# Kernel optimization log

Measured on AMD Instinct MI355X. Metric: run time of the kernel, lower is better.

## Reference

```python
import jax, jax.numpy as jnp
import numpy as np

B, S, H, I, E, K = 1, 2048, 1024, 2048, 8, 2


def setup_inputs() -> dict:
    key = jax.random.key(0)
    k0, k1, k2, k3, k4 = jax.random.split(key, 5)
    x = jax.random.normal(k0, (B, S, H), dtype=jnp.float32)
    Wg = jax.random.normal(k1, (H, E), dtype=jnp.float32) * 0.02   # gate (no bias)
    W1 = jax.random.normal(k2, (E, H, I), dtype=jnp.float32) * 0.02  # expert up
    W3 = jax.random.normal(k3, (E, H, I), dtype=jnp.float32) * 0.02  # expert gate
    W2 = jax.random.normal(k4, (E, I, H), dtype=jnp.float32) * 0.02  # expert down
    return {"x": x, "Wg": Wg, "W1": W1, "W2": W2, "W3": W3}


def reference(x, Wg, W1, W2, W3):
    b, s, h = x.shape
    e = Wg.shape[1]
    xf = x.reshape(-1, h)                      # (T, H)
    T = xf.shape[0]

    # Router: top-2 logits, softmax over the 2 selected logits (fp32), cast back.
    logits = xf @ Wg                           # (T, E)
    top_vals, top_idx = jax.lax.top_k(logits, K)
    rw = jax.nn.softmax(top_vals.astype(jnp.float32), axis=-1).astype(x.dtype)  # (T, K)

    # Dense per-expert combine weight: w[t, e] = routing weight if expert e selected, else 0.
    w = jnp.zeros((T, e), dtype=x.dtype).at[jnp.arange(T)[:, None], top_idx].add(rw)

    # Expert MLPs computed for all experts, zero-weighted tokens contribute nothing
    # (mathematically identical to the gather/MLP/scatter-add in the torch loop).
    up = jnp.einsum('th,ehi->tei', xf, W1)     # (T, E, I)
    gate = jnp.einsum('th,ehi->tei', xf, W3)   # (T, E, I)
    act = jax.nn.silu(up) * gate               # (T, E, I)
    out = jnp.einsum('tei,eih,te->th', act, W2, w)  # (T, H)
    return out.reshape(b, s, h)
```

## Files before the change

kernel.cpp:

```cpp
#include <hip/hip_runtime.h>
#include <math.h>

#define NUM_TOK 2048
#define HDIM 1024
#define IDIM 2048
#define NEXP 8
#define MAX_ROWS 5120
#define NTM 40

typedef __attribute__((ext_vector_type(8))) short bf16x8;
typedef __attribute__((ext_vector_type(4))) float f32x4;

#define OFF_IDX   0u
#define OFF_RW    16384u
#define OFF_CNT   32768u
#define OFF_SEG   32832u
#define OFF_ROWS  33024u
#define OFF_POS   53504u
#define OFF_XB    131072u
#define OFF_W1T   8388608u
#define OFF_W3T   41943040u
#define OFF_W2T   75497472u
#define OFF_ACT   109051904u
#define OFF_SO    8388608u

__device__ __forceinline__ unsigned short f2bf(float f) {
  union { float f; unsigned u; } v; v.f = f;
  unsigned r = v.u + 0x7FFF + ((v.u >> 16) & 1);
  return (unsigned short)(r >> 16);
}

__device__ __forceinline__ void gld16(const void* g, void* l) {
  __builtin_amdgcn_global_load_lds(
      (const __attribute__((address_space(1))) void*)g,
      (__attribute__((address_space(3))) void*)l, 16, 0, 0);
}

__global__ void __launch_bounds__(256, 4)
k_prep(const float* __restrict__ W1, const float* __restrict__ W3,
       const float* __restrict__ W2,
       unsigned short* __restrict__ W1T,
       unsigned short* __restrict__ W3T,
       unsigned short* __restrict__ W2T,
       const float* __restrict__ x, const float* __restrict__ wg,
       unsigned short* __restrict__ xb,
       int* __restrict__ idx, float* __restrict__ rw) {
  __shared__ unsigned D[64 * 129];
  const int z = blockIdx.z;
  const int t = threadIdx.x;
  if (z >= 24) {
    const int wave = t >> 6, lane = t & 63;
    const int id = blockIdx.x + 32 * blockIdx.y + 256 * (z - 24);
    const int tok = id * 4 + wave;
    if (tok >= NUM_TOK) return;
    const float2* __restrict__ xr = (const float2*)(x + (size_t)tok * HDIM);
    unsigned* __restrict__ xbr = (unsigned*)(xb + (size_t)tok * HDIM);
    float acc[8];
#pragma unroll
    for (int q = 0; q < 8; ++q) acc[q] = 0.f;
#pragma unroll
    for (int j = 0; j < 8; ++j) {
      const int h2 = lane + (j << 6);
      const float2 v = xr[h2];
      const float* wrow = wg + (size_t)h2 * 16;
      const float4 a0 = *(const float4*)(wrow);
      const float4 a1 = *(const float4*)(wrow + 4);
      const float4 b0 = *(const float4*)(wrow + 8);
      const float4 b1 = *(const float4*)(wrow + 12);
      acc[0] = fmaf(v.x, a0.x, fmaf(v.y, b0.x, acc[0]));
      acc[1] = fmaf(v.x, a0.y, fmaf(v.y, b0.y, acc[1]));
      acc[2] = fmaf(v.x, a0.z, fmaf(v.y, b0.z, acc[2]));
      acc[3] = fmaf(v.x, a0.w, fmaf(v.y, b0.w, acc[3]));
      acc[4] = fmaf(v.x, a1.x, fmaf(v.y, b1.x, acc[4]));
      acc[5] = fmaf(v.x, a1.y, fmaf(v.y, b1.y, acc[5]));
      acc[6] = fmaf(v.x, a1.z, fmaf(v.y, b1.z, acc[6]));
      acc[7] = fmaf(v.x, a1.w, fmaf(v.y, b1.w, acc[7]));
      xbr[h2] = (unsigned)f2bf(v.x) | ((unsigned)f2bf(v.y) << 16);
    }
#pragma unroll
    for (int q = 0; q < 8; ++q) {
#pragma unroll
      for (int off = 32; off >= 1; off >>= 1)
        acc[q] += __shfl_xor(acc[q], off, 64);
    }
    if (lane == 0) {
      int i0 = 0; float v0 = acc[0];
#pragma unroll
      for (int q = 1; q < 8; ++q)
        if (acc[q] > v0) { v0 = acc[q]; i0 = q; }
      int i1 = -1; float v1 = -3.4e38f;
#pragma unroll
      for (int q = 0; q < 8; ++q)
        if (q != i0 && acc[q] > v1) { v1 = acc[q]; i1 = q; }
      const float e1 = expf(v1 - v0);
      const float inv = 1.f / (1.f + e1);
      idx[2 * tok] = i0; idx[2 * tok + 1] = i1;
      rw[2 * tok] = inv; rw[2 * tok + 1] = e1 * inv;
    }
    return;
  }
  const float* src; unsigned short* dst; int R, C, eidx;
  if (z < 8)       { src = W1; dst = W1T; R = HDIM; C = IDIM; eidx = z; }
  else if (z < 16) { src = W3; dst = W3T; R = HDIM; C = IDIM; eidx = z - 8; }
  else             { src = W2; dst = W2T; R = IDIM; C = HDIM; eidx = z - 16; }
  const int r0 = blockIdx.y * 256;
  const int c0 = blockIdx.x * 64;
  if (r0 >= R || c0 >= C) return;
  const size_t base = (size_t)eidx * R * C;
  const int c4 = (t & 15) * 4;
  const int r2a = t >> 4;
  float4 va[4][2][2];
#pragma unroll
  for (int p = 0; p < 4; ++p)
#pragma unroll
    for (int h = 0; h < 2; ++h) {
      const int r = r0 + p * 64 + 2 * (r2a + 16 * h);
      va[p][h][0] = *(const float4*)(src + base + (size_t)r * C + c0 + c4);
      va[p][h][1] = *(const float4*)(src + base + (size_t)(r + 1) * C + c0 + c4);
    }
  __builtin_amdgcn_sched_barrier(0);
#pragma unroll
  for (int p = 0; p < 4; ++p)
#pragma unroll
    for (int h = 0; h < 2; ++h) {
      const int r2 = p * 32 + r2a + 16 * h;
      const float4 v0 = va[p][h][0], v1 = va[p][h][1];
      const float a0[4] = {v0.x, v0.y, v0.z, v0.w};
      const float a1[4] = {v1.x, v1.y, v1.z, v1.w};
#pragma unroll
      for (int q = 0; q < 4; ++q)
        D[(c4 + q) * 129 + r2] = (unsigned)f2bf(a0[q]) | ((unsigned)f2bf(a1[q]) << 16);
    }
  __syncthreads();
  const int rq = (t & 31) * 4;
#pragma unroll
  for (int g = 0; g < 8; ++g) {
    const int c = (t >> 5) + g * 8;
    uint4 u;
    u.x = D[c * 129 + rq];
    u.y = D[c * 129 + rq + 1];
    u.z = D[c * 129 + rq + 2];
    u.w = D[c * 129 + rq + 3];
    *(uint4*)(dst + base + (size_t)(c0 + c) * R + r0 + rq * 2) = u;
  }
}

__global__ void k_segscatter(const int* __restrict__ idx, int* __restrict__ seg,
                             int* __restrict__ rowsv, int* __restrict__ pos) {
  __shared__ int hist[NEXP], cur[NEXP], sseg[NEXP];
  const int tid = threadIdx.x;
  if (tid < NEXP) { hist[tid] = 0; cur[tid] = 0; }
  __syncthreads();
  for (int s = tid; s < 2 * NUM_TOK; s += 256) atomicAdd(&hist[idx[s]], 1);
  for (int r = tid; r < MAX_ROWS; r += 256) rowsv[r] = -1;
  __syncthreads();
  if (tid == 0) {
    int s = 0;
    for (int q = 0; q < NEXP; ++q) {
      seg[q] = s; sseg[q] = s;
      s += ((hist[q] + 127) / 128) * 128;
    }
    seg[NEXP] = s;
  }
  __syncthreads();
  for (int s = tid; s < 2 * NUM_TOK; s += 256) {
    const int e = idx[s];
    const int p = atomicAdd(&cur[e], 1);
    const int rr = sseg[e] + p;
    rowsv[rr] = s;
    pos[s] = rr;
  }
}

__launch_bounds__(256, 2)
__global__ void k_gemm1(const unsigned short* __restrict__ xb,
                        const unsigned short* __restrict__ W1T,
                        const unsigned short* __restrict__ W3T,
                        const int* __restrict__ seg, const int* __restrict__ rowsv,
                        unsigned short* __restrict__ act) {
  __shared__ __align__(16) unsigned short As[2][128 * 32];
  __shared__ __align__(16) unsigned short Bs[2][128 * 32];
  const int tid = threadIdx.x;
  const int w = tid >> 6, l = tid & 63;
  const int m0 = blockIdx.y * 128;
  const int total = seg[NEXP];
  if (m0 >= total) return;
  int e = 0;
#pragma unroll
  for (int q = 1; q < NEXP; ++q) if (m0 >= seg[q]) e = q;
  const int n0 = blockIdx.x * 64;

  const int swzst = ((l & 3) ^ ((l >> 3) & 3)) * 8;
  size_t aOff[2], bOff[2];
#pragma unroll
  for (int q = 0; q < 2; ++q) {
    const int r = rowsv[m0 + w * 32 + q * 16 + (l >> 2)];
    const int tk = (r < 0) ? 0 : (r >> 1);
    aOff[q] = (size_t)tk * HDIM + swzst;
    bOff[q] = ((size_t)e * IDIM + n0 + (w & 1) * 32 + q * 16 + (l >> 2)) * HDIM + swzst;
  }
  const unsigned short* __restrict__ WT = (w < 2) ? W1T : W3T;

  f32x4 acc[2][8];
#pragma unroll
  for (int m = 0; m < 2; ++m)
#pragma unroll
    for (int nf = 0; nf < 8; ++nf) acc[m][nf] = (f32x4)0.f;

  auto stage = [&](int buf, int k0) {
#pragma unroll
    for (int q = 0; q < 2; ++q) {
      gld16(xb + aOff[q] + k0, &As[buf][(w * 32 + q * 16) * 32]);
      gld16(WT + bOff[q] + k0, &Bs[buf][(w * 32 + q * 16) * 32]);
    }
  };

  stage(0, 0);
  __syncthreads();
  const int rslot = ((l >> 4) ^ ((l >> 1) & 3)) * 8;
  const int arow = (w * 32 + (l & 15)) * 32 + rslot;
  for (int t = 0; t < HDIM / 32; ++t) {
    const int cur = t & 1;
    if (t + 1 < HDIM / 32) stage(cur ^ 1, (t + 1) * 32);
    const bf16x8 a0 = *(const bf16x8*)&As[cur][arow];
    const bf16x8 a1 = *(const bf16x8*)&As[cur][arow + 16 * 32];
#pragma unroll
    for (int nf = 0; nf < 8; ++nf) {
      const bf16x8 b = *(const bf16x8*)&Bs[cur][(nf * 16 + (l & 15)) * 32 + rslot];
      acc[0][nf] = __builtin_amdgcn_mfma_f32_16x16x32_bf16(a0, b, acc[0][nf], 0, 0, 0);
      acc[1][nf] = __builtin_amdgcn_mfma_f32_16x16x32_bf16(a1, b, acc[1][nf], 0, 0, 0);
    }
    __syncthreads();
  }
  const int rbase = m0 + w * 32 + (l >> 4) * 4;
  const int cbase = n0 + (l & 15);
#pragma unroll
  for (int m = 0; m < 2; ++m)
#pragma unroll
    for (int p = 0; p < 4; ++p) {
      const f32x4 up = acc[m][p];
      const f32x4 gt = acc[m][p + 4];
#pragma unroll
      for (int r = 0; r < 4; ++r) {
        const float u = up[r];
        const float s = (u / (1.f + expf(-u))) * gt[r];
        act[(size_t)(rbase + m * 16 + r) * IDIM + cbase + p * 16] = f2bf(s);
      }
    }
}

__launch_bounds__(256, 2)
__global__ void k_gemm2(const unsigned short* __restrict__ act,
                        const unsigned short* __restrict__ W2T,
                        const int* __restrict__ seg,
                        float* __restrict__ so) {
  __shared__ __align__(16) unsigned short As[2][128 * 32];
  __shared__ __align__(16) unsigned short Bs[2][128 * 32];
  const int tid = threadIdx.x;
  const int w = tid >> 6, l = tid & 63;
  const int m0 = blockIdx.y * 128;
  const int total = seg[NEXP];
  if (m0 >= total) return;
  int e = 0;
#pragma unroll
  for (int q = 1; q < NEXP; ++q) if (m0 >= seg[q]) e = q;
  const int n0 = blockIdx.x * 128;
  const int swz = ((tid & 3) ^ ((tid >> 3) & 3)) * 8;
  size_t aOff[2], bOff[2];
#pragma unroll
  for (int q = 0; q < 2; ++q) {
    aOff[q] = (size_t)(m0 + q * 64 + (tid >> 2)) * IDIM + swz;
    bOff[q] = ((size_t)e * HDIM + n0 + q * 64 + (tid >> 2)) * IDIM + swz;
  }

  f32x4 acc[2][8];
#pragma unroll
  for (int mf = 0; mf < 2; ++mf)
#pragma unroll
    for (int nf = 0; nf < 8; ++nf) acc[mf][nf] = (f32x4)0.f;

  auto stage = [&](int buf, int k0) {
#pragma unroll
    for (int q = 0; q < 2; ++q) {
      gld16(act + aOff[q] + k0, &As[buf][(q * 64 + (tid >> 2)) * 32 + (tid & 3) * 8]);
      gld16(W2T + bOff[q] + k0, &Bs[buf][(q * 64 + (tid >> 2)) * 32 + (tid & 3) * 8]);
    }
  };

  stage(0, 0);
  __syncthreads();
  const int rslot = ((l >> 4) ^ ((l >> 1) & 3)) * 8;
  const int arow = (w * 32 + (l & 15)) * 32 + rslot;
  for (int t = 0; t < IDIM / 32; ++t) {
    const int cur = t & 1;
    if (t + 1 < IDIM / 32) stage(cur ^ 1, (t + 1) * 32);
    const bf16x8 a0 = *(const bf16x8*)&As[cur][arow];
    const bf16x8 a1 = *(const bf16x8*)&As[cur][arow + 16 * 32];
#pragma unroll
    for (int nf = 0; nf < 8; ++nf) {
      const bf16x8 b = *(const bf16x8*)&Bs[cur][(nf * 16 + (l & 15)) * 32 + rslot];
      acc[0][nf] = __builtin_amdgcn_mfma_f32_16x16x32_bf16(a0, b, acc[0][nf], 0, 0, 0);
      acc[1][nf] = __builtin_amdgcn_mfma_f32_16x16x32_bf16(a1, b, acc[1][nf], 0, 0, 0);
    }
    __syncthreads();
  }
  const int rbase = m0 + w * 32 + (l >> 4) * 4;
  const int cbase = n0 + (l & 15);
#pragma unroll
  for (int mf = 0; mf < 2; ++mf)
#pragma unroll
    for (int nf = 0; nf < 8; ++nf)
#pragma unroll
      for (int r = 0; r < 4; ++r)
        so[(size_t)(rbase + mf * 16 + r) * HDIM + cbase + nf * 16] = acc[mf][nf][r];
}

__global__ void k_combine(const float* __restrict__ so, const int* __restrict__ pos,
                          const float* __restrict__ rw, float* __restrict__ out) {
  const int t = blockIdx.x, i = threadIdx.x;
  const int p0 = pos[2 * t], p1 = pos[2 * t + 1];
  const float w0 = rw[2 * t], w1 = rw[2 * t + 1];
  const float4 a = ((const float4*)(so + (size_t)p0 * HDIM))[i];
  const float4 b = ((const float4*)(so + (size_t)p1 * HDIM))[i];
  float4 o;
  o.x = w0 * a.x + w1 * b.x;
  o.y = w0 * a.y + w1 * b.y;
  o.z = w0 * a.z + w1 * b.z;
  o.w = w0 * a.w + w1 * b.w;
  ((float4*)(out + (size_t)t * HDIM))[i] = o;
}

extern "C" void kernel_launch(void* const* d_in, const int* in_sizes, int n_in,
                              void* d_out, int out_size, void* d_ws, size_t ws_size,
                              hipStream_t stream) {
  const float* x  = (const float*)d_in[0];
  const float* Wg = (const float*)d_in[1];
  const float* W1 = (const float*)d_in[2];
  const float* W2 = (const float*)d_in[3];
  const float* W3 = (const float*)d_in[4];
  float* out = (float*)d_out;
  char* ws = (char*)d_ws;
  int*   idx  = (int*)(ws + OFF_IDX);
  float* rw   = (float*)(ws + OFF_RW);
  int*   seg  = (int*)(ws + OFF_SEG);
  int*   rowsv= (int*)(ws + OFF_ROWS);
  int*   pos  = (int*)(ws + OFF_POS);
  unsigned short* xb  = (unsigned short*)(ws + OFF_XB);
  unsigned short* W1T = (unsigned short*)(ws + OFF_W1T);
  unsigned short* W3T = (unsigned short*)(ws + OFF_W3T);
  unsigned short* W2T = (unsigned short*)(ws + OFF_W2T);
  unsigned short* act = (unsigned short*)(ws + OFF_ACT);
  float* so = (float*)(ws + OFF_SO);

  k_prep<<<dim3(32, 8, 26), 256, 0, stream>>>(W1, W3, W2, W1T, W3T, W2T,
                                              x, Wg, xb, idx, rw);
  k_segscatter<<<1, 256, 0, stream>>>(idx, seg, rowsv, pos);
  k_gemm1<<<dim3(IDIM / 64, NTM), 256, 0, stream>>>(xb, W1T, W3T, seg, rowsv, act);
  k_gemm2<<<dim3(HDIM / 128, NTM), 256, 0, stream>>>(act, W2T, seg, so);
  k_combine<<<NUM_TOK, 256, 0, stream>>>(so, pos, rw, out);
}
```

Baseline: 186.8 us.

## Fuse fp32-to-bf16 weight conversion into GEMM B-tile staging, drop prep transpose

Removes the separate prep pass that converted and transposed all expert weights to bf16 in workspace. Both GEMMs now read fp32 weights directly into registers, pack them to bf16 and write them into a swizzled, transposed LDS layout while the MFMAs on the current buffer run. The router becomes its own small kernel. This avoids writing and re-reading about 100 MB of bf16 weights, at the cost of each GEMM block reading fp32 weights redundantly across M-tiles, more VALU and LDS-store work in the inner loop, and more register pressure.

```diff
diff --git a/kernel.cpp b/kernel.cpp
--- a/kernel.cpp
+++ b/kernel.cpp
@@ -13,14 +13,10 @@
 
 #define OFF_IDX   0u
 #define OFF_RW    16384u
-#define OFF_CNT   32768u
 #define OFF_SEG   32832u
 #define OFF_ROWS  33024u
 #define OFF_POS   53504u
 #define OFF_XB    131072u
-#define OFF_W1T   8388608u
-#define OFF_W3T   41943040u
-#define OFF_W2T   75497472u
 #define OFF_ACT   109051904u
 #define OFF_SO    8388608u
 
@@ -30,118 +26,65 @@
   return (unsigned short)(r >> 16);
 }
 
+__device__ __forceinline__ unsigned pk2(float lo, float hi) {
+  return (unsigned)f2bf(lo) | ((unsigned)f2bf(hi) << 16);
+}
+
 __device__ __forceinline__ void gld16(const void* g, void* l) {
   __builtin_amdgcn_global_load_lds(
       (const __attribute__((address_space(1))) void*)g,
       (__attribute__((address_space(3))) void*)l, 16, 0, 0);
 }
 
-__global__ void __launch_bounds__(256, 4)
-k_prep(const float* __restrict__ W1, const float* __restrict__ W3,
-       const float* __restrict__ W2,
-       unsigned short* __restrict__ W1T,
-       unsigned short* __restrict__ W3T,
-       unsigned short* __restrict__ W2T,
-       const float* __restrict__ x, const float* __restrict__ wg,
-       unsigned short* __restrict__ xb,
-       int* __restrict__ idx, float* __restrict__ rw) {
-  __shared__ unsigned D[64 * 129];
-  const int z = blockIdx.z;
-  const int t = threadIdx.x;
-  if (z >= 24) {
-    const int wave = t >> 6, lane = t & 63;
-    const int id = blockIdx.x + 32 * blockIdx.y + 256 * (z - 24);
-    const int tok = id * 4 + wave;
-    if (tok >= NUM_TOK) return;
-    const float2* __restrict__ xr = (const float2*)(x + (size_t)tok * HDIM);
-    unsigned* __restrict__ xbr = (unsigned*)(xb + (size_t)tok * HDIM);
-    float acc[8];
-#pragma unroll
-    for (int q = 0; q < 8; ++q) acc[q] = 0.f;
-#pragma unroll
-    for (int j = 0; j < 8; ++j) {
-      const int h2 = lane + (j << 6);
-      const float2 v = xr[h2];
-      const float* wrow = wg + (size_t)h2 * 16;
-      const float4 a0 = *(const float4*)(wrow);
-      const float4 a1 = *(const float4*)(wrow + 4);
-      const float4 b0 = *(const float4*)(wrow + 8);
-      const float4 b1 = *(const float4*)(wrow + 12);
-      acc[0] = fmaf(v.x, a0.x, fmaf(v.y, b0.x, acc[0]));
-      acc[1] = fmaf(v.x, a0.y, fmaf(v.y, b0.y, acc[1]));
-      acc[2] = fmaf(v.x, a0.z, fmaf(v.y, b0.z, acc[2]));
-      acc[3] = fmaf(v.x, a0.w, fmaf(v.y, b0.w, acc[3]));
-      acc[4] = fmaf(v.x, a1.x, fmaf(v.y, b1.x, acc[4]));
-      acc[5] = fmaf(v.x, a1.y, fmaf(v.y, b1.y, acc[5]));
-      acc[6] = fmaf(v.x, a1.z, fmaf(v.y, b1.z, acc[6]));
-      acc[7] = fmaf(v.x, a1.w, fmaf(v.y, b1.w, acc[7]));
-      xbr[h2] = (unsigned)f2bf(v.x) | ((unsigned)f2bf(v.y) << 16);
-    }
-#pragma unroll
-    for (int q = 0; q < 8; ++q) {
-#pragma unroll
-      for (int off = 32; off >= 1; off >>= 1)
-        acc[q] += __shfl_xor(acc[q], off, 64);
-    }
-    if (lane == 0) {
-      int i0 = 0; float v0 = acc[0];
-#pragma unroll
-      for (int q = 1; q < 8; ++q)
-        if (acc[q] > v0) { v0 = acc[q]; i0 = q; }
-      int i1 = -1; float v1 = -3.4e38f;
-#pragma unroll
-      for (int q = 0; q < 8; ++q)
-        if (q != i0 && acc[q] > v1) { v1 = acc[q]; i1 = q; }
-      const float e1 = expf(v1 - v0);
-      const float inv = 1.f / (1.f + e1);
-      idx[2 * tok] = i0; idx[2 * tok + 1] = i1;
-      rw[2 * tok] = inv; rw[2 * tok + 1] = e1 * inv;
-    }
-    return;
-  }
-  const float* src; unsigned short* dst; int R, C, eidx;
-  if (z < 8)       { src = W1; dst = W1T; R = HDIM; C = IDIM; eidx = z; }
-  else if (z < 16) { src = W3; dst = W3T; R = HDIM; C = IDIM; eidx = z - 8; }
-  else             { src = W2; dst = W2T; R = IDIM; C = HDIM; eidx = z - 16; }
-  const int r0 = blockIdx.y * 256;
-  const int c0 = blockIdx.x * 64;
-  if (r0 >= R || c0 >= C) return;
-  const size_t base = (size_t)eidx * R * C;
-  const int c4 = (t & 15) * 4;
-  const int r2a = t >> 4;
-  float4 va[4][2][2];
-#pragma unroll
-  for (int p = 0; p < 4; ++p)
-#pragma unroll
-    for (int h = 0; h < 2; ++h) {
-      const int r = r0 + p * 64 + 2 * (r2a + 16 * h);
-      va[p][h][0] = *(const float4*)(src + base + (size_t)r * C + c0 + c4);
-      va[p][h][1] = *(const float4*)(src + base + (size_t)(r + 1) * C + c0 + c4);
-    }
-  __builtin_amdgcn_sched_barrier(0);
-#pragma unroll
-  for (int p = 0; p < 4; ++p)
-#pragma unroll
-    for (int h = 0; h < 2; ++h) {
-      const int r2 = p * 32 + r2a + 16 * h;
-      const float4 v0 = va[p][h][0], v1 = va[p][h][1];
-      const float a0[4] = {v0.x, v0.y, v0.z, v0.w};
-      const float a1[4] = {v1.x, v1.y, v1.z, v1.w};
-#pragma unroll
-      for (int q = 0; q < 4; ++q)
-        D[(c4 + q) * 129 + r2] = (unsigned)f2bf(a0[q]) | ((unsigned)f2bf(a1[q]) << 16);
-    }
-  __syncthreads();
-  const int rq = (t & 31) * 4;
-#pragma unroll
-  for (int g = 0; g < 8; ++g) {
-    const int c = (t >> 5) + g * 8;
-    uint4 u;
-    u.x = D[c * 129 + rq];
-    u.y = D[c * 129 + rq + 1];
-    u.z = D[c * 129 + rq + 2];
-    u.w = D[c * 129 + rq + 3];
-    *(uint4*)(dst + base + (size_t)(c0 + c) * R + r0 + rq * 2) = u;
+
+__global__ void k_router(const float* __restrict__ x, const float* __restrict__ wg,
+                         unsigned short* __restrict__ xb,
+                         int* __restrict__ idx, float* __restrict__ rw) {
+  const int wave = threadIdx.x >> 6, lane = threadIdx.x & 63;
+  const int t = blockIdx.x * 4 + wave;
+  const float2* __restrict__ xr = (const float2*)(x + (size_t)t * HDIM);
+  unsigned* __restrict__ xbr = (unsigned*)(xb + (size_t)t * HDIM);
+  float acc[8];
+#pragma unroll
+  for (int q = 0; q < 8; ++q) acc[q] = 0.f;
+#pragma unroll
+  for (int j = 0; j < 8; ++j) {
+    const int h2 = lane + (j << 6);
+    const float2 v = xr[h2];
+    const float* wrow = wg + (size_t)h2 * 16;
+    const float4 a0 = *(const float4*)(wrow);
+    const float4 a1 = *(const float4*)(wrow + 4);
+    const float4 b0 = *(const float4*)(wrow + 8);
+    const float4 b1 = *(const float4*)(wrow + 12);
+    acc[0] = fmaf(v.x, a0.x, fmaf(v.y, b0.x, acc[0]));
+    acc[1] = fmaf(v.x, a0.y, fmaf(v.y, b0.y, acc[1]));
+    acc[2] = fmaf(v.x, a0.z, fmaf(v.y, b0.z, acc[2]));
+    acc[3] = fmaf(v.x, a0.w, fmaf(v.y, b0.w, acc[3]));
+    acc[4] = fmaf(v.x, a1.x, fmaf(v.y, b1.x, acc[4]));
+    acc[5] = fmaf(v.x, a1.y, fmaf(v.y, b1.y, acc[5]));
+    acc[6] = fmaf(v.x, a1.z, fmaf(v.y, b1.z, acc[6]));
+    acc[7] = fmaf(v.x, a1.w, fmaf(v.y, b1.w, acc[7]));
+    xbr[h2] = pk2(v.x, v.y);
+  }
+#pragma unroll
+  for (int q = 0; q < 8; ++q) {
+#pragma unroll
+    for (int off = 32; off >= 1; off >>= 1)
+      acc[q] += __shfl_xor(acc[q], off, 64);
+  }
+  if (lane == 0) {
+    int i0 = 0; float v0 = acc[0];
+#pragma unroll
+    for (int q = 1; q < 8; ++q)
+      if (acc[q] > v0) { v0 = acc[q]; i0 = q; }
+    int i1 = -1; float v1 = -3.4e38f;
+#pragma unroll
+    for (int q = 0; q < 8; ++q)
+      if (q != i0 && acc[q] > v1) { v1 = acc[q]; i1 = q; }
+    const float e1 = expf(v1 - v0);
+    const float inv = 1.f / (1.f + e1);
+    idx[2 * t] = i0; idx[2 * t + 1] = i1;
+    rw[2 * t] = inv; rw[2 * t + 1] = e1 * inv;
   }
 }
 
@@ -174,8 +117,8 @@
 
 __launch_bounds__(256, 2)
 __global__ void k_gemm1(const unsigned short* __restrict__ xb,
-                        const unsigned short* __restrict__ W1T,
-                        const unsigned short* __restrict__ W3T,
+                        const float* __restrict__ W1f,
+                        const float* __restrict__ W3f,
                         const int* __restrict__ seg, const int* __restrict__ rowsv,
                         unsigned short* __restrict__ act) {
   __shared__ __align__(16) unsigned short As[2][128 * 32];
@@ -190,16 +133,45 @@
   for (int q = 1; q < NEXP; ++q) if (m0 >= seg[q]) e = q;
   const int n0 = blockIdx.x * 64;
 
-  const int swzst = ((l & 3) ^ ((l >> 3) & 3)) * 8;
-  size_t aOff[2], bOff[2];
+  const int swzA = ((l & 3) ^ ((l >> 4) & 3) ^ ((l >> 3) & 3)) * 8;
+  size_t aOff[2];
 #pragma unroll
   for (int q = 0; q < 2; ++q) {
     const int r = rowsv[m0 + w * 32 + q * 16 + (l >> 2)];
     const int tk = (r < 0) ? 0 : (r >> 1);
-    aOff[q] = (size_t)tk * HDIM + swzst;
-    bOff[q] = ((size_t)e * IDIM + n0 + (w & 1) * 32 + q * 16 + (l >> 2)) * HDIM + swzst;
-  }
-  const unsigned short* __restrict__ WT = (w < 2) ? W1T : W3T;
+    aOff[q] = (size_t)tk * HDIM + swzA;
+  }
+  const int kk = tid >> 4;
+  const int ng = tid & 15;
+  const size_t bBase = (size_t)e * HDIM * IDIM + (size_t)(2 * kk) * IDIM + n0 + ng * 4;
+  float4 u0, u1, g0, g1;
+  auto loadB = [&](int k0) {
+    const size_t b = bBase + (size_t)k0 * IDIM;
+    u0 = *(const float4*)(W1f + b);
+    u1 = *(const float4*)(W1f + b + IDIM);
+    g0 = *(const float4*)(W3f + b);
+    g1 = *(const float4*)(W3f + b + IDIM);
+  };
+  auto writeB = [&](int buf) {
+    unsigned* Bd = (unsigned*)&Bs[buf][0];
+    const float a0[4] = {u0.x, u0.y, u0.z, u0.w};
+    const float a1[4] = {u1.x, u1.y, u1.z, u1.w};
+    const float c0[4] = {g0.x, g0.y, g0.z, g0.w};
+    const float c1[4] = {g1.x, g1.y, g1.z, g1.w};
+#pragma unroll
+    for (int i = 0; i < 4; ++i) {
+      const int r = ng * 4 + i;
+      const int f = ((r >> 2) & 3) ^ ((r >> 1) & 3);
+      const int d = (((kk >> 2) ^ f) << 2) + (kk & 3);
+      Bd[r * 16 + d]        = pk2(a0[i], a1[i]);
+      Bd[(r + 64) * 16 + d] = pk2(c0[i], c1[i]);
+    }
+  };
+  auto stageA = [&](int buf, int k0) {
+#pragma unroll
+    for (int q = 0; q < 2; ++q)
+      gld16(xb + aOff[q] + k0, &As[buf][(w * 32 + q * 16) * 32]);
+  };
 
   f32x4 acc[2][8];
 #pragma unroll
@@ -207,21 +179,18 @@
 #pragma unroll
     for (int nf = 0; nf < 8; ++nf) acc[m][nf] = (f32x4)0.f;
 
-  auto stage = [&](int buf, int k0) {
-#pragma unroll
-    for (int q = 0; q < 2; ++q) {
-      gld16(xb + aOff[q] + k0, &As[buf][(w * 32 + q * 16) * 32]);
-      gld16(WT + bOff[q] + k0, &Bs[buf][(w * 32 + q * 16) * 32]);
-    }
-  };
-
-  stage(0, 0);
-  __syncthreads();
-  const int rslot = ((l >> 4) ^ ((l >> 1) & 3)) * 8;
+  stageA(0, 0);
+  loadB(0);
+  writeB(0);
+  __syncthreads();
+
+  const int rslot = ((l >> 4) ^ ((l >> 2) & 3) ^ ((l >> 1) & 3)) * 8;
   const int arow = (w * 32 + (l & 15)) * 32 + rslot;
-  for (int t = 0; t < HDIM / 32; ++t) {
+  const int NT = HDIM / 32;
+  for (int t = 0; t < NT; ++t) {
     const int cur = t & 1;
-    if (t + 1 < HDIM / 32) stage(cur ^ 1, (t + 1) * 32);
+    if (t + 1 < NT) { stageA(cur ^ 1, (t + 1) * 32); loadB((t + 1) * 32); }
+    __builtin_amdgcn_sched_barrier(0);
     const bf16x8 a0 = *(const bf16x8*)&As[cur][arow];
     const bf16x8 a1 = *(const bf16x8*)&As[cur][arow + 16 * 32];
 #pragma unroll
@@ -230,6 +199,7 @@
       acc[0][nf] = __builtin_amdgcn_mfma_f32_16x16x32_bf16(a0, b, acc[0][nf], 0, 0, 0);
       acc[1][nf] = __builtin_amdgcn_mfma_f32_16x16x32_bf16(a1, b, acc[1][nf], 0, 0, 0);
     }
+    if (t + 1 < NT) writeB(cur ^ 1);
     __syncthreads();
   }
   const int rbase = m0 + w * 32 + (l >> 4) * 4;
@@ -251,7 +221,7 @@
 
 __launch_bounds__(256, 2)
 __global__ void k_gemm2(const unsigned short* __restrict__ act,
-                        const unsigned short* __restrict__ W2T,
+                        const float* __restrict__ W2f,
                         const int* __restrict__ seg,
                         float* __restrict__ so) {
   __shared__ __align__(16) unsigned short As[2][128 * 32];
@@ -265,13 +235,45 @@
 #pragma unroll
   for (int q = 1; q < NEXP; ++q) if (m0 >= seg[q]) e = q;
   const int n0 = blockIdx.x * 128;
-  const int swz = ((tid & 3) ^ ((tid >> 3) & 3)) * 8;
-  size_t aOff[2], bOff[2];
-#pragma unroll
-  for (int q = 0; q < 2; ++q) {
-    aOff[q] = (size_t)(m0 + q * 64 + (tid >> 2)) * IDIM + swz;
-    bOff[q] = ((size_t)e * HDIM + n0 + q * 64 + (tid >> 2)) * IDIM + swz;
-  }
+
+  const int swzA = ((tid & 3) ^ ((tid >> 4) & 3) ^ ((tid >> 3) & 3)) * 8;
+  size_t aOff[2];
+#pragma unroll
+  for (int q = 0; q < 2; ++q)
+    aOff[q] = (size_t)(m0 + q * 64 + (tid >> 2)) * IDIM + swzA;
+
+  const int kk = tid >> 4;
+  const int ng = tid & 15;
+  const size_t bBase = (size_t)e * IDIM * HDIM + (size_t)(2 * kk) * HDIM + n0 + ng * 4;
+  float4 v0[2], v1[2];
+  auto loadB = [&](int k0) {
+#pragma unroll
+    for (int q = 0; q < 2; ++q) {
+      const size_t b = bBase + (size_t)k0 * HDIM + q * 64;
+      v0[q] = *(const float4*)(W2f + b);
+      v1[q] = *(const float4*)(W2f + b + HDIM);
+    }
+  };
+  auto writeB = [&](int buf) {
+    unsigned* Bd = (unsigned*)&Bs[buf][0];
+#pragma unroll
+    for (int q = 0; q < 2; ++q) {
+      const float a0[4] = {v0[q].x, v0[q].y, v0[q].z, v0[q].w};
+      const float a1[4] = {v1[q].x, v1[q].y, v1[q].z, v1[q].w};
+#pragma unroll
+      for (int i = 0; i < 4; ++i) {
+        const int rm = ng * 4 + i;
+        const int f = ((rm >> 2) & 3) ^ ((rm >> 1) & 3);
+        const int d = (((kk >> 2) ^ f) << 2) + (kk & 3);
+        Bd[(q * 64 + rm) * 16 + d] = pk2(a0[i], a1[i]);
+      }
+    }
+  };
+  auto stageA = [&](int buf, int k0) {
+#pragma unroll
+    for (int q = 0; q < 2; ++q)
+      gld16(act + aOff[q] + k0, &As[buf][(q * 64 + (tid >> 2)) * 32]);
+  };
 
   f32x4 acc[2][8];
 #pragma unroll
@@ -279,21 +281,18 @@
 #pragma unroll
     for (int nf = 0; nf < 8; ++nf) acc[mf][nf] = (f32x4)0.f;
 
-  auto stage = [&](int buf, int k0) {
-#pragma unroll
-    for (int q = 0; q < 2; ++q) {
-      gld16(act + aOff[q] + k0, &As[buf][(q * 64 + (tid >> 2)) * 32 + (tid & 3) * 8]);
-      gld16(W2T + bOff[q] + k0, &Bs[buf][(q * 64 + (tid >> 2)) * 32 + (tid & 3) * 8]);
-    }
-  };
-
-  stage(0, 0);
-  __syncthreads();
-  const int rslot = ((l >> 4) ^ ((l >> 1) & 3)) * 8;
+  stageA(0, 0);
+  loadB(0);
+  writeB(0);
+  __syncthreads();
+
+  const int rslot = ((l >> 4) ^ ((l >> 2) & 3) ^ ((l >> 1) & 3)) * 8;
   const int arow = (w * 32 + (l & 15)) * 32 + rslot;
-  for (int t = 0; t < IDIM / 32; ++t) {
+  const int NT = IDIM / 32;
+  for (int t = 0; t < NT; ++t) {
     const int cur = t & 1;
-    if (t + 1 < IDIM / 32) stage(cur ^ 1, (t + 1) * 32);
+    if (t + 1 < NT) { stageA(cur ^ 1, (t + 1) * 32); loadB((t + 1) * 32); }
+    __builtin_amdgcn_sched_barrier(0);
     const bf16x8 a0 = *(const bf16x8*)&As[cur][arow];
     const bf16x8 a1 = *(const bf16x8*)&As[cur][arow + 16 * 32];
 #pragma unroll
@@ -302,6 +301,7 @@
       acc[0][nf] = __builtin_amdgcn_mfma_f32_16x16x32_bf16(a0, b, acc[0][nf], 0, 0, 0);
       acc[1][nf] = __builtin_amdgcn_mfma_f32_16x16x32_bf16(a1, b, acc[1][nf], 0, 0, 0);
     }
+    if (t + 1 < NT) writeB(cur ^ 1);
     __syncthreads();
   }
   const int rbase = m0 + w * 32 + (l >> 4) * 4;
@@ -346,16 +346,12 @@
   int*   rowsv= (int*)(ws + OFF_ROWS);
   int*   pos  = (int*)(ws + OFF_POS);
   unsigned short* xb  = (unsigned short*)(ws + OFF_XB);
-  unsigned short* W1T = (unsigned short*)(ws + OFF_W1T);
-  unsigned short* W3T = (unsigned short*)(ws + OFF_W3T);
-  unsigned short* W2T = (unsigned short*)(ws + OFF_W2T);
   unsigned short* act = (unsigned short*)(ws + OFF_ACT);
   float* so = (float*)(ws + OFF_SO);
 
-  k_prep<<<dim3(32, 8, 26), 256, 0, stream>>>(W1, W3, W2, W1T, W3T, W2T,
-                                              x, Wg, xb, idx, rw);
+  k_router<<<NUM_TOK / 4, 256, 0, stream>>>(x, Wg, xb, idx, rw);
   k_segscatter<<<1, 256, 0, stream>>>(idx, seg, rowsv, pos);
-  k_gemm1<<<dim3(IDIM / 64, NTM), 256, 0, stream>>>(xb, W1T, W3T, seg, rowsv, act);
-  k_gemm2<<<dim3(HDIM / 128, NTM), 256, 0, stream>>>(act, W2T, seg, so);
+  k_gemm1<<<dim3(IDIM / 64, NTM), 256, 0, stream>>>(xb, W1, W3, seg, rowsv, act);
+  k_gemm2<<<dim3(HDIM / 128, NTM), 256, 0, stream>>>(act, W2, seg, so);
   k_combine<<<NUM_TOK, 256, 0, stream>>>(so, pos, rw, out);
 }
```

New measurement: 166.5 us. 10.9% less time.
